# Kernel tuning notes

Hardware: AMD Instinct MI355X
Metric: run time of the kernel (lower is better)

## Reference

```python
import jax, jax.numpy as jnp
import numpy as np

N = 100000   # nodes
E = 300000   # directed edges (avg degree 3, molecular graphs)
G = 4000     # molecules in the batch
IN = 9
HID = 128
HEADS = 4
NEG_SLOPE = 0.2


def setup_inputs() -> dict:
    key = jax.random.key(0)
    ks = jax.random.split(key, 12)
    x = jax.random.normal(ks[0], (N, IN), dtype=jnp.float32)
    edge_index = jax.random.randint(ks[1], (2, E), 0, N, dtype=jnp.int32)
    batch = jnp.sort(jax.random.randint(ks[2], (N,), 0, G, dtype=jnp.int32))
    s = 0.1  # keep activations in a sane range
    W1 = jax.random.normal(ks[3], (IN, HEADS * HID), dtype=jnp.float32) * s
    a_src1 = jax.random.normal(ks[4], (HEADS, HID), dtype=jnp.float32) * s
    a_dst1 = jax.random.normal(ks[5], (HEADS, HID), dtype=jnp.float32) * s
    b1 = jax.random.normal(ks[6], (HEADS * HID,), dtype=jnp.float32) * s
    W2 = jax.random.normal(ks[7], (HEADS * HID, HID), dtype=jnp.float32) * s
    a_src2 = jax.random.normal(ks[8], (1, HID), dtype=jnp.float32) * s
    a_dst2 = jax.random.normal(ks[9], (1, HID), dtype=jnp.float32) * s
    b2 = jax.random.normal(ks[10], (HID,), dtype=jnp.float32) * s
    return {"x": x, "edge_index": edge_index, "batch": batch,
            "W1": W1, "a_src1": a_src1, "a_dst1": a_dst1, "b1": b1,
            "W2": W2, "a_src2": a_src2, "a_dst2": a_dst2, "b2": b2}


def _gat_conv(x, edge_index, W, a_src, a_dst, b, heads, out_ch, concat):
    """PyG GATConv: linear proj, per-edge leaky-relu attention logits,
    segment softmax over destination nodes, scatter-add aggregation.
    add_self_loops=True (PyG default)."""
    n = x.shape[0]
    loops = jnp.arange(n, dtype=edge_index.dtype)
    src = jnp.concatenate([edge_index[0], loops])
    dst = jnp.concatenate([edge_index[1], loops])

    h = (x @ W).reshape(n, heads, out_ch)                  # [N, H, C]
    alpha_s = jnp.einsum('nhc,hc->nh', h, a_src)           # [N, H]
    alpha_d = jnp.einsum('nhc,hc->nh', h, a_dst)           # [N, H]

    logits = jax.nn.leaky_relu(alpha_s[src] + alpha_d[dst], NEG_SLOPE)  # [Etot, H]
    # numerically stable segment softmax over incoming edges of each dst
    m = jax.ops.segment_max(logits, dst, num_segments=n)   # [N, H] (finite: self-loops)
    e = jnp.exp(logits - m[dst])
    z = jax.ops.segment_sum(e, dst, num_segments=n)
    alpha = e / (z[dst] + 1e-16)                           # [Etot, H]

    msg = h[src] * alpha[:, :, None]                       # [Etot, H, C]
    out = jax.ops.segment_sum(msg, dst, num_segments=n)    # [N, H, C]
    if concat:
        out = out.reshape(n, heads * out_ch)
    else:
        out = out.mean(axis=1)
    return out + b


def reference(x, edge_index, batch, W1, a_src1, a_dst1, b1, W2, a_src2, a_dst2, b2):
    h = jax.nn.elu(_gat_conv(x, edge_index, W1, a_src1, a_dst1, b1, HEADS, HID, True))
    h = jax.nn.elu(_gat_conv(h, edge_index, W2, a_src2, a_dst2, b2, 1, HID, True))
    # global mean pool per graph
    sums = jax.ops.segment_sum(h, batch, num_segments=G)   # [G, HID]
    cnt = jax.ops.segment_sum(jnp.ones((h.shape[0],), h.dtype), batch, num_segments=G)
    return sums / jnp.maximum(cnt, 1.0)[:, None]
```

## Files before the change

### kernel.cpp

```cpp
#include <hip/hip_runtime.h>

#define N_NODES 100000
#define N_EDGES 300000
#define N_GRAPHS 4000
#define CAP 32

typedef float f32x4 __attribute__((ext_vector_type(4)));
typedef __bf16 bf16x8 __attribute__((ext_vector_type(8)));
typedef __bf16 bf16x2 __attribute__((ext_vector_type(2)));

static const size_t OFF_XA    = 0;
static const size_t OFF_AD4   = OFF_XA + (size_t)N_NODES * 16;
static const size_t OFF_P2B   = OFF_AD4 + (size_t)N_NODES * 4;
static const size_t OFF_ASAD2 = OFF_P2B + (size_t)N_NODES * 64;
static const size_t OFF_WSB   = OFF_ASAD2 + (size_t)N_NODES * 2;
static const size_t OFF_GST   = OFF_WSB + 32768;
static const size_t OFF_INT   = OFF_GST + 4096;

#define PRE_NODE_END 391
#define PRE_PACKB_END 455
#define PRE_DEG_END 846
#define PRE_GST_END 862

__device__ __forceinline__ float lrelu(float x) { return x < 0.f ? 0.2f * x : x; }
__device__ __forceinline__ float elu(float x)   { return x > 0.f ? x : __expf(x) - 1.f; }

__global__ __launch_bounds__(256) void k_pre(
    const float* __restrict__ x, const float* __restrict__ W1,
    const float* __restrict__ a_src1, const float* __restrict__ a_dst1,
    const float* __restrict__ W2, const int* __restrict__ batch,
    float* __restrict__ xa, float* __restrict__ ad4,
    __bf16* __restrict__ wsB, int* __restrict__ deg, int* __restrict__ gstart) {
    int b = blockIdx.x, tid = threadIdx.x;
    if (b < PRE_NODE_END) {
        __shared__ float wf[72];
        if (tid < 72) {
            int isd = tid / 36, r = tid % 36, k = r / 4, h = r % 4;
            const float* a = isd ? a_dst1 : a_src1;
            float s = 0.f;
            for (int c = 0; c < 128; c++) s += W1[k * 512 + h * 128 + c] * a[h * 128 + c];
            wf[tid] = s;
        }
        __syncthreads();
        int n = b * 256 + tid;
        if (n >= N_NODES) return;
        float xv[9];
#pragma unroll
        for (int k = 0; k < 9; k++) xv[k] = x[n * 9 + k];
        float as[4], ad[4];
#pragma unroll
        for (int h = 0; h < 4; h++) {
            float s = 0.f, d = 0.f;
#pragma unroll
            for (int k = 0; k < 9; k++) {
                s += xv[k] * wf[k * 4 + h];
                d += xv[k] * wf[36 + k * 4 + h];
            }
            as[h] = s; ad[h] = d;
        }
        f32x4* xp = (f32x4*)(xa + (size_t)n * 16);
        xp[0] = (f32x4){xv[0], xv[1], xv[2], xv[3]};
        xp[1] = (f32x4){xv[4], xv[5], xv[6], xv[7]};
        xp[2] = (f32x4){xv[8], as[0], as[1], as[2]};
        xp[3] = (f32x4){as[3], 0.f, 0.f, 0.f};
        *(f32x4*)(ad4 + (size_t)n * 4) = (f32x4){ad[0], ad[1], ad[2], ad[3]};
    } else if (b < PRE_PACKB_END) {
        int t = (b - PRE_NODE_END) * 256 + tid;
#pragma unroll
        for (int m = 0; m < 4; m++) {
            int idx = t * 4 + m;
            int k = idx >> 7, nn = idx & 127;
            wsB[(size_t)nn * 512 + k] = (__bf16)W2[(size_t)k * 128 + nn];
        }
    } else if (b < PRE_DEG_END) {
        int idx = (b - PRE_PACKB_END) * 256 + tid;
        if (idx < N_NODES) deg[idx] = 0;
    } else {
        int g = (b - PRE_DEG_END) * 256 + tid;
        if (g > N_GRAPHS) return;
        int lo = 0, hi = N_NODES;
        while (lo < hi) { int mid = (lo + hi) >> 1; if (batch[mid] < g) lo = mid + 1; else hi = mid; }
        gstart[g] = lo;
    }
}

__global__ void k_bucket(const int* __restrict__ ei, int* __restrict__ deg,
                         int* __restrict__ bucket) {
    int e = blockIdx.x * 256 + threadIdx.x;
    if (e >= N_EDGES) return;
    int s = ei[e], d = ei[N_EDGES + e];
    int slot = atomicAdd(&deg[d], 1);
    if (slot < CAP) bucket[d * CAP + slot] = s;
}

__global__ __launch_bounds__(512, 6) void k_gemm(
    const float* __restrict__ xa, const float* __restrict__ ad4,
    const int* __restrict__ deg, const int* __restrict__ bucket,
    const float* __restrict__ W1, const float* __restrict__ b1,
    const __bf16* __restrict__ wsB,
    const float* __restrict__ a_src2, const float* __restrict__ a_dst2,
    __bf16* __restrict__ p2b, float* __restrict__ asad2) {
    __shared__ __bf16 As[64 * 256];
    __shared__ float W1s[9 * 260];
    __shared__ __bf16 AgT[64 * 72];
    float* red2 = (float*)AgT;
    const int tid = threadIdx.x;
    const int lane = tid & 63;
    const int w = tid >> 6;
    const int i = lane & 15;
    const int q = lane >> 4;
    const int m0 = blockIdx.x * 64;

    for (int idx = tid; idx < 2304; idx += 512) {
        int k = idx >> 8, j = idx & 255;
        W1s[k * 260 + j] = W1[k * 512 + j];
    }

    {
        int nh = tid >> 1, sub = tid & 1;
        int r = nh >> 2, h = nh & 3;
        int n = m0 + r;
        float acc[9] = {};
        float z = 0.f;
        bool valid = (n < N_NODES);
        if (valid) {
            float ad = ad4[(size_t)n * 4 + h];
            int dg = deg[n];
            if (dg > CAP) dg = CAP;
            if (sub == 0) {
                const f32x4* xp = (const f32x4*)(xa + (size_t)n * 16);
                f32x4 v0 = xp[0], v1 = xp[1], v2 = xp[2], v3 = xp[3];
                float asl = (h == 0) ? v2.y : (h == 1) ? v2.z : (h == 2) ? v2.w : v3.x;
                float e = __expf(lrelu(asl + ad));
                z += e;
                acc[0] += e * v0.x; acc[1] += e * v0.y; acc[2] += e * v0.z; acc[3] += e * v0.w;
                acc[4] += e * v1.x; acc[5] += e * v1.y; acc[6] += e * v1.z; acc[7] += e * v1.w;
                acc[8] += e * v2.x;
            }
            for (int j = sub; j < dg; j += 2) {
                int src = bucket[n * CAP + j];
                const f32x4* xp = (const f32x4*)(xa + (size_t)src * 16);
                f32x4 v0 = xp[0], v1 = xp[1], v2 = xp[2], v3 = xp[3];
                float asl = (h == 0) ? v2.y : (h == 1) ? v2.z : (h == 2) ? v2.w : v3.x;
                float e = __expf(lrelu(asl + ad));
                z += e;
                acc[0] += e * v0.x; acc[1] += e * v0.y; acc[2] += e * v0.z; acc[3] += e * v0.w;
                acc[4] += e * v1.x; acc[5] += e * v1.y; acc[6] += e * v1.z; acc[7] += e * v1.w;
                acc[8] += e * v2.x;
            }
        }
        z += __shfl_xor(z, 1);
#pragma unroll
        for (int k = 0; k < 9; k++) acc[k] += __shfl_xor(acc[k], 1);
        if (sub == 0) {
            float inv = valid ? 1.f / z : 0.f;
            bf16x8 p0;
#pragma unroll
            for (int k = 0; k < 8; k++) p0[k] = (__bf16)(acc[k] * inv);
            __bf16* dst = AgT + r * 72 + h * 16;
            *(bf16x8*)dst = p0;
            dst[8] = (__bf16)(acc[8] * inv);
        }
    }
    __syncthreads();

    f32x4 acc[4];
#pragma unroll
    for (int r = 0; r < 4; r++) acc[r] = (f32x4){0.f, 0.f, 0.f, 0.f};

    const int row = tid & 63;
    const int kg = __builtin_amdgcn_readfirstlane(tid >> 6);
    const int rt_p1 = row >> 4, il = row & 15;
    const __bf16* bcol = wsB + (size_t)(w * 16 + i) * 512 + q * 8;

#pragma unroll
    for (int half = 0; half < 2; half++) {
        bf16x8 breg[8];
#pragma unroll
        for (int kc = 0; kc < 8; kc++)
            breg[kc] = *(const bf16x8*)(bcol + half * 256 + kc * 32);

        {
            int h = half * 2 + (kg >> 2);
            float ag[9];
            {
                bf16x8 a8 = *(const bf16x8*)&AgT[row * 72 + h * 16];
#pragma unroll
                for (int k = 0; k < 8; k++) ag[k] = (float)a8[k];
                ag[8] = (float)AgT[row * 72 + h * 16 + 8];
            }
#pragma unroll
            for (int c8 = 0; c8 < 4; c8++) {
                int jr = kg * 32 + c8 * 8;
                int j0 = half * 256 + jr;
                float o[8];
#pragma unroll
                for (int e = 0; e < 8; e++) o[e] = b1[j0 + e];
#pragma unroll
                for (int k = 0; k < 9; k++) {
                    f32x4 wa = *(const f32x4*)&W1s[k * 260 + jr];
                    f32x4 wb = *(const f32x4*)&W1s[k * 260 + jr + 4];
                    o[0] += ag[k] * wa.x; o[1] += ag[k] * wa.y;
                    o[2] += ag[k] * wa.z; o[3] += ag[k] * wa.w;
                    o[4] += ag[k] * wb.x; o[5] += ag[k] * wb.y;
                    o[6] += ag[k] * wb.z; o[7] += ag[k] * wb.w;
                }
                bf16x8 pk;
#pragma unroll
                for (int e = 0; e < 8; e++) pk[e] = (__bf16)elu(o[e]);
                *(bf16x8*)&As[(rt_p1 * 8 + kg) * 512 + (c8 * 16 + il) * 8] = pk;
            }
        }
        __syncthreads();

        if (half == 0) {
            for (int idx = tid; idx < 2304; idx += 512) {
                int k = idx >> 8, j = idx & 255;
                W1s[k * 260 + j] = W1[k * 512 + 256 + j];
            }
        }

#pragma unroll
        for (int kc = 0; kc < 8; kc++) {
#pragma unroll
            for (int rt = 0; rt < 4; rt++) {
                bf16x8 af = *(const bf16x8*)&As[(rt * 8 + kc) * 512 + lane * 8];
                acc[rt] = __builtin_amdgcn_mfma_f32_16x16x32_bf16(af, breg[kc], acc[rt], 0, 0, 0);
            }
        }
        __syncthreads();
    }

    float as2 = a_src2[w * 16 + i];
    float ad2 = a_dst2[w * 16 + i];
#pragma unroll
    for (int rt = 0; rt < 4; rt++) {
#pragma unroll
        for (int qq = 0; qq < 4; qq++) {
            int r2 = rt * 16 + q * 4 + qq;
            float v = acc[rt][qq];
            if (m0 + r2 < N_NODES)
                p2b[(size_t)(m0 + r2) * 128 + w * 16 + i] = (__bf16)v;
            float s = v * as2, d = v * ad2;
#pragma unroll
            for (int off = 1; off < 16; off <<= 1) {
                s += __shfl_xor(s, off);
                d += __shfl_xor(d, off);
            }
            if (i == 0) {
                red2[r2 * 16 + w * 2] = s;
                red2[r2 * 16 + w * 2 + 1] = d;
            }
        }
    }
    __syncthreads();
    if (tid < 128) {
        int r2 = tid >> 1, cc = tid & 1;
        float sum = 0.f;
#pragma unroll
        for (int ww = 0; ww < 8; ww++) sum += red2[r2 * 16 + ww * 2 + cc];
        if (m0 + r2 < N_NODES) asad2[(size_t)(m0 + r2) * 2 + cc] = sum;
    }
}

__global__ void k_agg2_pool(const __bf16* __restrict__ p2b, const float* __restrict__ asad2,
                            const int* __restrict__ deg, const int* __restrict__ bucket,
                            const float* __restrict__ b2, const int* __restrict__ gstart,
                            float* __restrict__ out) {
    int g = (blockIdx.x * 256 + threadIdx.x) >> 6;
    g = __builtin_amdgcn_readfirstlane(g);
    if (g >= N_GRAPHS) return;
    int lane = threadIdx.x & 63;
    int s0n = gstart[g], e0n = gstart[g + 1];
    float b2a = b2[2 * lane], b2b = b2[2 * lane + 1];
    float g0 = 0.f, g1 = 0.f;
    for (int n = s0n; n < e0n; n++) {
        float ad = asad2[n * 2 + 1];
        float e = __expf(lrelu(asad2[n * 2] + ad));
        float z = e;
        bf16x2 v = ((const bf16x2*)(p2b + (size_t)n * 128))[lane];
        float a0 = e * (float)v.x;
        float a1 = e * (float)v.y;
        int dg = deg[n];
        if (dg > CAP) dg = CAP;
        for (int j = 0; j < dg; j += 4) {
            int s0 = bucket[n * CAP + j];
            int s1 = bucket[n * CAP + min(j + 1, dg - 1)];
            int s2 = bucket[n * CAP + min(j + 2, dg - 1)];
            int s3 = bucket[n * CAP + min(j + 3, dg - 1)];
            float l0 = asad2[s0 * 2], l1 = asad2[s1 * 2];
            float l2 = asad2[s2 * 2], l3 = asad2[s3 * 2];
            bf16x2 w0 = ((const bf16x2*)(p2b + (size_t)s0 * 128))[lane];
            bf16x2 w1 = ((const bf16x2*)(p2b + (size_t)s1 * 128))[lane];
            bf16x2 w2 = ((const bf16x2*)(p2b + (size_t)s2 * 128))[lane];
            bf16x2 w3 = ((const bf16x2*)(p2b + (size_t)s3 * 128))[lane];
            float e0 = __expf(lrelu(l0 + ad));
            float e1 = (j + 1 < dg) ? __expf(lrelu(l1 + ad)) : 0.f;
            float e2 = (j + 2 < dg) ? __expf(lrelu(l2 + ad)) : 0.f;
            float e3 = (j + 3 < dg) ? __expf(lrelu(l3 + ad)) : 0.f;
            z += e0 + e1 + e2 + e3;
            a0 += e0 * (float)w0.x + e1 * (float)w1.x + e2 * (float)w2.x + e3 * (float)w3.x;
            a1 += e0 * (float)w0.y + e1 * (float)w1.y + e2 * (float)w2.y + e3 * (float)w3.y;
        }
        float inv = 1.f / z;
        g0 += elu(a0 * inv + b2a);
        g1 += elu(a1 * inv + b2b);
    }
    int cnt = e0n - s0n;
    float ic = 1.f / (float)(cnt > 0 ? cnt : 1);
    out[(size_t)g * 128 + 2 * lane] = g0 * ic;
    out[(size_t)g * 128 + 2 * lane + 1] = g1 * ic;
}

extern "C" void kernel_launch(void* const* d_in, const int* in_sizes, int n_in,
                              void* d_out, int out_size, void* d_ws, size_t ws_size,
                              hipStream_t stream) {
    const float* x       = (const float*)d_in[0];
    const int*   ei      = (const int*)d_in[1];
    const int*   batch   = (const int*)d_in[2];
    const float* W1      = (const float*)d_in[3];
    const float* a_src1  = (const float*)d_in[4];
    const float* a_dst1  = (const float*)d_in[5];
    const float* b1      = (const float*)d_in[6];
    const float* W2      = (const float*)d_in[7];
    const float* a_src2  = (const float*)d_in[8];
    const float* a_dst2  = (const float*)d_in[9];
    const float* b2      = (const float*)d_in[10];
    float* out = (float*)d_out;

    float* wsf   = (float*)d_ws;
    float* xa    = wsf + OFF_XA;
    float* ad4   = wsf + OFF_AD4;
    __bf16* p2b  = (__bf16*)(wsf + OFF_P2B);
    float* asad2 = wsf + OFF_ASAD2;
    __bf16* wsB  = (__bf16*)(wsf + OFF_WSB);
    int* gstart  = (int*)(wsf + OFF_GST);
    int* wsi    = (int*)(wsf + OFF_INT);
    int* deg    = wsi;
    int* bucket = wsi + N_NODES;

    k_pre<<<PRE_GST_END, 256, 0, stream>>>(x, W1, a_src1, a_dst1, W2, batch,
                                           xa, ad4, wsB, deg, gstart);
    k_bucket<<<(N_EDGES + 255) / 256, 256, 0, stream>>>(ei, deg, bucket);
    k_gemm<<<(N_NODES + 63) / 64, 512, 0, stream>>>(xa, ad4, deg, bucket, W1, b1,
                                                    wsB, a_src2, a_dst2, p2b, asad2);
    k_agg2_pool<<<(N_GRAPHS * 64) / 256, 256, 0, stream>>>(
        p2b, asad2, deg, bucket, b2, gstart, out);
}
```

Before: 233.4 us.

## Split layer-2 aggregation into per-node kernel plus separate pooling; read W1 from global

The fused per-graph layer-2 aggregation and mean-pool kernel is split in two. One kernel runs a wavefront per node and writes a bf16 hidden row to a new workspace buffer. A second kernel then mean-pools those rows per graph. This exposes 100k wavefronts instead of 4k serial per-graph loops, which should raise parallelism and latency hiding for the gather, at the cost of an extra intermediate write/read and a kernel launch. Separately, the GEMM kernel drops the LDS staging of W1 and reads W1 directly from global memory (cached), removing a sync-dependent copy and freeing LDS, with red2 getting its own shared array.

Measured after the change: 218.1 us. 6.6% less time.

```diff
diff --git a/kernel.cpp b/kernel.cpp
--- a/kernel.cpp
+++ b/kernel.cpp
@@ -13,7 +13,8 @@
 static const size_t OFF_AD4   = OFF_XA + (size_t)N_NODES * 16;
 static const size_t OFF_P2B   = OFF_AD4 + (size_t)N_NODES * 4;
 static const size_t OFF_ASAD2 = OFF_P2B + (size_t)N_NODES * 64;
-static const size_t OFF_WSB   = OFF_ASAD2 + (size_t)N_NODES * 2;
+static const size_t OFF_H3B   = OFF_ASAD2 + (size_t)N_NODES * 2;
+static const size_t OFF_WSB   = OFF_H3B + (size_t)N_NODES * 64;
 static const size_t OFF_GST   = OFF_WSB + 32768;
 static const size_t OFF_INT   = OFF_GST + 4096;
 
@@ -101,20 +102,14 @@
     const float* __restrict__ a_src2, const float* __restrict__ a_dst2,
     __bf16* __restrict__ p2b, float* __restrict__ asad2) {
     __shared__ __bf16 As[64 * 256];
-    __shared__ float W1s[9 * 260];
     __shared__ __bf16 AgT[64 * 72];
-    float* red2 = (float*)AgT;
+    __shared__ float red2[64 * 16];
     const int tid = threadIdx.x;
     const int lane = tid & 63;
     const int w = tid >> 6;
     const int i = lane & 15;
     const int q = lane >> 4;
     const int m0 = blockIdx.x * 64;
-
-    for (int idx = tid; idx < 2304; idx += 512) {
-        int k = idx >> 8, j = idx & 255;
-        W1s[k * 260 + j] = W1[k * 512 + j];
-    }
 
     {
         int nh = tid >> 1, sub = tid & 1;
@@ -191,19 +186,15 @@
             }
 #pragma unroll
             for (int c8 = 0; c8 < 4; c8++) {
-                int jr = kg * 32 + c8 * 8;
-                int j0 = half * 256 + jr;
+                int j0 = half * 256 + kg * 32 + c8 * 8;
                 float o[8];
 #pragma unroll
                 for (int e = 0; e < 8; e++) o[e] = b1[j0 + e];
 #pragma unroll
                 for (int k = 0; k < 9; k++) {
-                    f32x4 wa = *(const f32x4*)&W1s[k * 260 + jr];
-                    f32x4 wb = *(const f32x4*)&W1s[k * 260 + jr + 4];
-                    o[0] += ag[k] * wa.x; o[1] += ag[k] * wa.y;
-                    o[2] += ag[k] * wa.z; o[3] += ag[k] * wa.w;
-                    o[4] += ag[k] * wb.x; o[5] += ag[k] * wb.y;
-                    o[6] += ag[k] * wb.z; o[7] += ag[k] * wb.w;
+                    const float* wp = &W1[k * 512 + j0];
+#pragma unroll
+                    for (int e = 0; e < 8; e++) o[e] += ag[k] * wp[e];
                 }
                 bf16x8 pk;
 #pragma unroll
@@ -212,13 +203,6 @@
             }
         }
         __syncthreads();
-
-        if (half == 0) {
-            for (int idx = tid; idx < 2304; idx += 512) {
-                int k = idx >> 8, j = idx & 255;
-                W1s[k * 260 + j] = W1[k * 512 + 256 + j];
-            }
-        }
 
 #pragma unroll
         for (int kc = 0; kc < 8; kc++) {
@@ -263,53 +247,64 @@
     }
 }
 
-__global__ void k_agg2_pool(const __bf16* __restrict__ p2b, const float* __restrict__ asad2,
-                            const int* __restrict__ deg, const int* __restrict__ bucket,
-                            const float* __restrict__ b2, const int* __restrict__ gstart,
-                            float* __restrict__ out) {
+__global__ void k_agg2(const __bf16* __restrict__ p2b, const float* __restrict__ asad2,
+                       const int* __restrict__ deg, const int* __restrict__ bucket,
+                       const float* __restrict__ b2, __bf16* __restrict__ h3b) {
+    int n = (blockIdx.x * 256 + threadIdx.x) >> 6;
+    n = __builtin_amdgcn_readfirstlane(n);
+    if (n >= N_NODES) return;
+    int lane = threadIdx.x & 63;
+    float ad = asad2[n * 2 + 1];
+    float e = __expf(lrelu(asad2[n * 2] + ad));
+    float z = e;
+    bf16x2 v = ((const bf16x2*)(p2b + (size_t)n * 128))[lane];
+    float a0 = e * (float)v.x;
+    float a1 = e * (float)v.y;
+    int dg = deg[n];
+    if (dg > CAP) dg = CAP;
+    for (int j = 0; j < dg; j += 4) {
+        int s0 = bucket[n * CAP + j];
+        int s1 = bucket[n * CAP + min(j + 1, dg - 1)];
+        int s2 = bucket[n * CAP + min(j + 2, dg - 1)];
+        int s3 = bucket[n * CAP + min(j + 3, dg - 1)];
+        float l0 = asad2[s0 * 2], l1 = asad2[s1 * 2];
+        float l2 = asad2[s2 * 2], l3 = asad2[s3 * 2];
+        bf16x2 w0 = ((const bf16x2*)(p2b + (size_t)s0 * 128))[lane];
+        bf16x2 w1 = ((const bf16x2*)(p2b + (size_t)s1 * 128))[lane];
+        bf16x2 w2 = ((const bf16x2*)(p2b + (size_t)s2 * 128))[lane];
+        bf16x2 w3 = ((const bf16x2*)(p2b + (size_t)s3 * 128))[lane];
+        float e0 = __expf(lrelu(l0 + ad));
+        float e1 = (j + 1 < dg) ? __expf(lrelu(l1 + ad)) : 0.f;
+        float e2 = (j + 2 < dg) ? __expf(lrelu(l2 + ad)) : 0.f;
+        float e3 = (j + 3 < dg) ? __expf(lrelu(l3 + ad)) : 0.f;
+        z += e0 + e1 + e2 + e3;
+        a0 += e0 * (float)w0.x + e1 * (float)w1.x + e2 * (float)w2.x + e3 * (float)w3.x;
+        a1 += e0 * (float)w0.y + e1 * (float)w1.y + e2 * (float)w2.y + e3 * (float)w3.y;
+    }
+    float inv = 1.f / z;
+    bf16x2 o;
+    o.x = (__bf16)elu(a0 * inv + b2[2 * lane]);
+    o.y = (__bf16)elu(a1 * inv + b2[2 * lane + 1]);
+    ((bf16x2*)(h3b + (size_t)n * 128))[lane] = o;
+}
+
+__global__ void k_pool(const __bf16* __restrict__ h3b, const int* __restrict__ gstart,
+                       float* __restrict__ out) {
     int g = (blockIdx.x * 256 + threadIdx.x) >> 6;
     g = __builtin_amdgcn_readfirstlane(g);
     if (g >= N_GRAPHS) return;
     int lane = threadIdx.x & 63;
-    int s0n = gstart[g], e0n = gstart[g + 1];
-    float b2a = b2[2 * lane], b2b = b2[2 * lane + 1];
-    float g0 = 0.f, g1 = 0.f;
-    for (int n = s0n; n < e0n; n++) {
-        float ad = asad2[n * 2 + 1];
-        float e = __expf(lrelu(asad2[n * 2] + ad));
-        float z = e;
-        bf16x2 v = ((const bf16x2*)(p2b + (size_t)n * 128))[lane];
-        float a0 = e * (float)v.x;
-        float a1 = e * (float)v.y;
-        int dg = deg[n];
-        if (dg > CAP) dg = CAP;
-        for (int j = 0; j < dg; j += 4) {
-            int s0 = bucket[n * CAP + j];
-            int s1 = bucket[n * CAP + min(j + 1, dg - 1)];
-            int s2 = bucket[n * CAP + min(j + 2, dg - 1)];
-            int s3 = bucket[n * CAP + min(j + 3, dg - 1)];
-            float l0 = asad2[s0 * 2], l1 = asad2[s1 * 2];
-            float l2 = asad2[s2 * 2], l3 = asad2[s3 * 2];
-            bf16x2 w0 = ((const bf16x2*)(p2b + (size_t)s0 * 128))[lane];
-            bf16x2 w1 = ((const bf16x2*)(p2b + (size_t)s1 * 128))[lane];
-            bf16x2 w2 = ((const bf16x2*)(p2b + (size_t)s2 * 128))[lane];
-            bf16x2 w3 = ((const bf16x2*)(p2b + (size_t)s3 * 128))[lane];
-            float e0 = __expf(lrelu(l0 + ad));
-            float e1 = (j + 1 < dg) ? __expf(lrelu(l1 + ad)) : 0.f;
-            float e2 = (j + 2 < dg) ? __expf(lrelu(l2 + ad)) : 0.f;
-            float e3 = (j + 3 < dg) ? __expf(lrelu(l3 + ad)) : 0.f;
-            z += e0 + e1 + e2 + e3;
-            a0 += e0 * (float)w0.x + e1 * (float)w1.x + e2 * (float)w2.x + e3 * (float)w3.x;
-            a1 += e0 * (float)w0.y + e1 * (float)w1.y + e2 * (float)w2.y + e3 * (float)w3.y;
-        }
-        float inv = 1.f / z;
-        g0 += elu(a0 * inv + b2a);
-        g1 += elu(a1 * inv + b2b);
-    }
-    int cnt = e0n - s0n;
-    float ic = 1.f / (float)(cnt > 0 ? cnt : 1);
-    out[(size_t)g * 128 + 2 * lane] = g0 * ic;
-    out[(size_t)g * 128 + 2 * lane + 1] = g1 * ic;
+    int s = gstart[g], e = gstart[g + 1];
+    float a0 = 0.f, a1 = 0.f;
+    for (int n = s; n < e; n++) {
+        bf16x2 v = ((const bf16x2*)(h3b + (size_t)n * 128))[lane];
+        a0 += (float)v.x;
+        a1 += (float)v.y;
+    }
+    int cnt = e - s;
+    float ic = (cnt > 0) ? 1.f / (float)cnt : 0.f;
+    out[(size_t)g * 128 + 2 * lane] = a0 * ic;
+    out[(size_t)g * 128 + 2 * lane + 1] = a1 * ic;
 }
 
 extern "C" void kernel_launch(void* const* d_in, const int* in_sizes, int n_in,
@@ -333,6 +328,7 @@
     float* ad4   = wsf + OFF_AD4;
     __bf16* p2b  = (__bf16*)(wsf + OFF_P2B);
     float* asad2 = wsf + OFF_ASAD2;
+    __bf16* h3b  = (__bf16*)(wsf + OFF_H3B);
     __bf16* wsB  = (__bf16*)(wsf + OFF_WSB);
     int* gstart  = (int*)(wsf + OFF_GST);
     int* wsi    = (int*)(wsf + OFF_INT);
@@ -344,6 +340,7 @@
     k_bucket<<<(N_EDGES + 255) / 256, 256, 0, stream>>>(ei, deg, bucket);
     k_gemm<<<(N_NODES + 63) / 64, 512, 0, stream>>>(xa, ad4, deg, bucket, W1, b1,
                                                     wsB, a_src2, a_dst2, p2b, asad2);
-    k_agg2_pool<<<(N_GRAPHS * 64) / 256, 256, 0, stream>>>(
-        p2b, asad2, deg, bucket, b2, gstart, out);
-}
+    k_agg2<<<((size_t)N_NODES * 64 + 255) / 256, 256, 0, stream>>>(
+        p2b, asad2, deg, bucket, b2, h3b);
+    k_pool<<<(N_GRAPHS * 64) / 256, 256, 0, stream>>>(h3b, gstart, out);
+}
```
